# Kernel tuning notes

Measured on AMD Instinct MI355X. Metric: run time of the kernel, lower is better.

Reference implementation:

```python
import jax, jax.numpy as jnp
import numpy as np

F, P, H, HEADS, C, NCLS = 18, 128, 256, 8, 32, 625
SCALES = (2, 4, 6)
MAX_ITER = 2  # self.max_iterations in the source


def _mhsa(x, Wq, bq, Wk, bk, Wv, bv, Wo, bo):
    # x: [B, S, H]. Adjacency mask is all-ones in the source (adjacency()
    # returns torch.ones), so the mask is a mathematical no-op and is omitted.
    B, S, _ = x.shape
    hd = H // HEADS
    q = (x @ Wq + bq).reshape(B, S, HEADS, hd)
    k = (x @ Wk + bk).reshape(B, S, HEADS, hd)
    v = (x @ Wv + bv).reshape(B, S, HEADS, hd)
    scores = jnp.einsum('bqhd,bkhd->bhqk', q, k) / jnp.sqrt(jnp.float32(hd))
    attn = jax.nn.softmax(scores, axis=-1)
    out = jnp.einsum('bhqk,bkhd->bqhd', attn, v).reshape(B, S, H)
    return out @ Wo + bo


def _temporal_locality(scale, emb, Wq, bq, Wk, bk, Wv, bv, Wo, bo):
    # Vectorized overlap-add version of the python loop over windows.
    nw = F - scale + 1
    idx = jnp.arange(nw)[:, None] + jnp.arange(scale)[None, :]   # [nw, scale]
    windows = emb[idx].reshape(nw, scale * P, H)                 # [nw, s*P, H]
    out = _mhsa(windows, Wq, bq, Wk, bk, Wv, bv, Wo, bo)
    out = out.reshape(nw * scale, P, H)
    gval = jnp.zeros((F, P, H), emb.dtype).at[idx.reshape(-1)].add(out)
    # overlap counts == the hardcoded norm_scale vectors for F=18
    counts = jnp.zeros((F,), emb.dtype).at[idx.reshape(-1)].add(1.0)
    return gval / counts[:, None, None]


def _forward(multiscale_embed, unary_W, unary_b, halt_W, halt_b, compat,
             mp_W, mp_b, cls_W, cls_b,
             mhsa_Wq, mhsa_bq, mhsa_Wk, mhsa_bk,
             mhsa_Wv, mhsa_bv, mhsa_Wo, mhsa_bo):
    context = jnp.zeros_like(multiscale_embed)                 # [F, P, H]
    ptn = jnp.zeros((F,), multiscale_embed.dtype)
    Rt = jnp.zeros_like(ptn)
    Nt = jnp.zeros_like(ptn)
    # unary potentials: [F, P, C] -> permute -> [P, F, C]
    marginal = (multiscale_embed @ unary_W + unary_b).transpose(1, 0, 2)
    inputs = multiscale_embed                                   # [F, P, H]
    for _ in range(MAX_ITER):
        # --- halting probability (ACT-style) ---
        p = jnp.mean(jax.nn.sigmoid(inputs @ halt_W + halt_b), axis=1)[:, 0]  # [F]
        run = (ptn < 1.0).astype(ptn.dtype)
        new_halted = (ptn + p * run > 0.99).astype(ptn.dtype) * run
        run = (ptn + p * run <= 0.99).astype(ptn.dtype) * run
        ptn = ptn + p * run
        Rt = Rt + new_halted * (1.0 - ptn)
        ptn = ptn + new_halted * Rt
        Nt = Nt + run + new_halted
        # --- message passing: multi-scale windowed self-attention ---
        g = jnp.zeros_like(inputs)
        for i, s in enumerate(SCALES):
            g = g + _temporal_locality(s, inputs,
                                       mhsa_Wq[i], mhsa_bq[i], mhsa_Wk[i], mhsa_bk[i],
                                       mhsa_Wv[i], mhsa_bv[i], mhsa_Wo[i], mhsa_bo[i])
        temporal = 0.25 * g                                     # [F, P, H]
        inputs_p = temporal.transpose(1, 0, 2)                  # [P, F, H]
        pairwise = inputs_p @ mp_W + mp_b                       # [P, F, C]
        # compatibility transform: the chunk/cat reshuffle is an identity
        # permutation; the math is out_k = sum_c compat[k,c] * pairwise[...,c]
        pairwise = jnp.einsum('pfc,kc->pfk', pairwise, compat)
        marginal = marginal - pairwise
        # --- transition function ---
        w = (p * run + new_halted * Rt)[:, None, None]          # [F,1,1]
        inputs = inputs_p.transpose(1, 0, 2)                    # [F, P, H]
        context = inputs * w + context * (1.0 - w)
    # --- cluster features ---
    # chunk/cat flattening uses index order p*F + f on both tensors
    m = jax.nn.softmax(marginal, axis=2).reshape(P * F, C)
    ctx = context.transpose(1, 0, 2).reshape(P * F, H)
    cluster_features = m.T @ ctx                                # [C, H]
    classes = jnp.sum(cluster_features, axis=0, keepdims=True) @ cls_W + cls_b
    return classes                                              # [1, NCLS]


def setup_inputs() -> dict:
    key = jax.random.key(0)
    ks = jax.random.split(key, 16)
    init = lambda k, shape: jax.random.normal(k, shape, dtype=jnp.float32) * 0.02
    return {
        'multiscale_embed': jax.random.normal(ks[0], (F, P, H), dtype=jnp.float32),
        'unary_W': init(ks[1], (H, C)),
        'unary_b': jnp.zeros((C,), jnp.float32),
        'halt_W': init(ks[2], (H, 1)),
        'halt_b': jnp.ones((1,), jnp.float32),  # bias filled with 1.0 in source
        'compat': -jnp.eye(C, dtype=jnp.float32),
        'mp_W': init(ks[3], (H, C)),
        'mp_b': jnp.zeros((C,), jnp.float32),
        'cls_W': init(ks[4], (H, NCLS)),
        'cls_b': jnp.zeros((NCLS,), jnp.float32),
        'mhsa_Wq': init(ks[5], (3, H, H)),
        'mhsa_bq': jnp.zeros((3, H), jnp.float32),
        'mhsa_Wk': init(ks[6], (3, H, H)),
        'mhsa_bk': jnp.zeros((3, H), jnp.float32),
        'mhsa_Wv': init(ks[7], (3, H, H)),
        'mhsa_bv': jnp.zeros((3, H), jnp.float32),
        'mhsa_Wo': init(ks[8], (3, H, H)),
        'mhsa_bo': jnp.zeros((3, H), jnp.float32),
        'labels': jax.random.randint(ks[9], (1,), 0, NCLS),
    }


def reference(multiscale_embed, unary_W, unary_b, halt_W, halt_b, compat,
              mp_W, mp_b, cls_W, cls_b,
              mhsa_Wq, mhsa_bq, mhsa_Wk, mhsa_bk,
              mhsa_Wv, mhsa_bv, mhsa_Wo, mhsa_bo, labels):
    del labels  # labels are not used in the forward math shown in the source
    return _forward(multiscale_embed, unary_W, unary_b, halt_W, halt_b, compat,
                    mp_W, mp_b, cls_W, cls_b,
                    mhsa_Wq, mhsa_bq, mhsa_Wk, mhsa_bk,
                    mhsa_Wv, mhsa_bv, mhsa_Wo, mhsa_bo)
```

## Files before the change

kernel.cpp:

```cpp
#include <hip/hip_runtime.h>
#include <hip/hip_bf16.h>

typedef __hip_bfloat16 bf16;

#define F 18
#define P 128
#define H 256
#define HEADS 8
#define HD 32
#define NCLS 625
#define FPH (F*P*H)
#define RPS 589824
#define NT16 144

#define OF_PTN    16
#define OF_RT     48
#define OF_W      80
#define OF_OSUM   128
#define OF_CTX    512
#define OF_FW     (OF_CTX + FPH)
#define WO2_HALTW 0
#define WO2_HALTB 256
#define WO2_CLSB  272
#define WO2_CLSW  912
#define WO2_BQ    160912
#define WO2_BK    161680
#define WO2_BV    162448
#define WO2_BO    163216
#define FW_TOTAL  163984
#define NF_TOTAL  (OF_FW + FW_TOTAL)

#define BB_WQT 0
#define BB_WKT 196608
#define BB_WVT 393216
#define BB_WOT 589824
#define BB_INP 786432
#define BB_QB  1376256
#define BB_KB  (BB_QB + 3*RPS)
#define BB_VT  (BB_KB + 3*RPS)
#define BB_AO  (BB_VT + 3*RPS)
#define BB_OB  (BB_AO + 3*RPS)
#define OB_ROWS0 0
#define OB_ROWS1 4352
#define OB_ROWS2 12032

typedef __attribute__((ext_vector_type(8))) short s8v;
typedef __attribute__((ext_vector_type(4))) short s4v;
typedef __attribute__((ext_vector_type(4))) float f4v;

__device__ __forceinline__ float b2f(bf16 x){ return __bfloat162float(x); }
__device__ __forceinline__ unsigned short f2bu(float x){
    union { __hip_bfloat16 h; unsigned short u; } cv; cv.h = __float2bfloat16(x); return cv.u;
}
__device__ __forceinline__ float bu2f(unsigned short u){
    union { unsigned int x; float f; } cv; cv.x = ((unsigned int)u) << 16; return cv.f;
}
__device__ __forceinline__ void b2x2(unsigned int u, float& a, float& b){
    union { unsigned int x; float f; } c1, c2;
    c1.x = u << 16; c2.x = u & 0xffff0000u; a = c1.f; b = c2.f;
}

#if __has_builtin(__builtin_amdgcn_cvt_pk_bf16_f32)
typedef __attribute__((ext_vector_type(2))) __bf16 bf2_t;
__device__ __forceinline__ unsigned int pk2(float a, float b){
    union { bf2_t v; unsigned int u; } cv;
    cv.v = __builtin_amdgcn_cvt_pk_bf16_f32(a, b);
    return cv.u;
}
#else
__device__ __forceinline__ unsigned int pk2(float a, float b){
    return (unsigned int)f2bu(a) | ((unsigned int)f2bu(b) << 16);
}
#endif

#if __has_builtin(__builtin_amdgcn_exp2f)
__device__ __forceinline__ float fexp2(float x){ return __builtin_amdgcn_exp2f(x); }
#else
__device__ __forceinline__ float fexp2(float x){ return exp2f(x); }
#endif

__device__ __forceinline__ int imin(int a,int b){ return a<b?a:b; }
__device__ __forceinline__ int imax(int a,int b){ return a>b?a:b; }

__device__ __forceinline__ int detect_bf16_block(const unsigned int* __restrict__ embw,
                                                 int* scnt)
{
    if (threadIdx.x == 0) *scnt = 0;
    __syncthreads();
    int c = 0;
    {
        unsigned int e = (embw[2*threadIdx.x] >> 7) & 0xffu;
        if (e >= 120u && e <= 130u) c++;
        e = (embw[2*threadIdx.x + 1] >> 7) & 0xffu;
        if (e >= 120u && e <= 130u) c++;
    }
    atomicAdd(scnt, c);
    __syncthreads();
    return (*scnt > 256) ? 1 : 0;
}

struct ConvArgs {
    const void* src[13];
    int mode[13];
    int n[13];
    int off[13];
};
__global__ __launch_bounds__(256) void k_convert(ConvArgs a,
        const unsigned int* __restrict__ embw,
        float* __restrict__ ws, bf16* __restrict__ bb)
{
    __shared__ int scnt;
    const int isbf = detect_bf16_block(embw, &scnt);
    int gid = blockIdx.x*256 + threadIdx.x;
#pragma unroll
    for (int t = 0; t < 13; ++t){
        if (gid < a.n[t]){
            float v = isbf ? b2f(((const bf16*)a.src[t])[gid])
                           : ((const float*)a.src[t])[gid];
            if (a.mode[t] == 0){
                ws[a.off[t] + gid] = v;
            } else if (a.mode[t] == 1){
                const int i = gid >> 16, rem = gid & 65535;
                const int k = rem >> 8, nn = rem & 255;
                bb[a.off[t] + (i << 16) + (nn << 8) + k] = __float2bfloat16(v);
            } else {
                bb[BB_INP + gid] = __float2bfloat16(v);
            }
            return;
        }
        gid -= a.n[t];
    }
}

__global__ __launch_bounds__(256) void k_qkv_mfma(const bf16* __restrict__ X,
        const bf16* __restrict__ WQT, const bf16* __restrict__ WKT,
        const bf16* __restrict__ WVT, const float* __restrict__ fw,
        bf16* __restrict__ qball, bf16* __restrict__ kball, bf16* __restrict__ vball)
{
    const int tid = threadIdx.x;
    if (blockIdx.z == 3){
        if (blockIdx.x >= F || blockIdx.y != 0) return;
        __shared__ float hw[H];
        __shared__ float red[256];
        float* ws = (float*)fw - OF_FW;
        const float* hW = fw + WO2_HALTW;
        const int f = blockIdx.x;
        hw[tid] = hW[tid];
        __syncthreads();
        float sg = 0.f;
        if (tid < P){
            const uint4* row = (const uint4*)(X + (size_t)(f*P + tid)*H);
            float acc = fw[WO2_HALTB];
#pragma unroll
            for (int i = 0; i < 16; ++i){
                const uint4 u = row[i];
                float a0,a1,a2,a3,a4,a5,a6,a7;
                b2x2(u.x,a0,a1); b2x2(u.y,a2,a3); b2x2(u.z,a4,a5); b2x2(u.w,a6,a7);
                const int b = i*16;
                acc = fmaf(a0,hw[b+0],acc); acc = fmaf(a1,hw[b+1],acc);
                acc = fmaf(a2,hw[b+2],acc); acc = fmaf(a3,hw[b+3],acc);
                acc = fmaf(a4,hw[b+4],acc); acc = fmaf(a5,hw[b+5],acc);
                acc = fmaf(a6,hw[b+6],acc); acc = fmaf(a7,hw[b+7],acc);
            }
            sg = 1.f/(1.f + __expf(-acc));
        }
        red[tid] = sg;
        __syncthreads();
        for (int s = 128; s > 0; s >>= 1){ if (tid < s) red[tid] += red[tid+s]; __syncthreads(); }
        if (tid == 0){
            float pf = red[0] * (1.f/P);
            float pt = ws[OF_PTN + f], rt = ws[OF_RT + f];
            float run  = (pt < 1.f) ? 1.f : 0.f;
            float cond = (pt + pf*run > 0.99f) ? 1.f : 0.f;
            float nh   = cond*run;
            run = (1.f - cond)*run;
            pt += pf*run;
            rt += nh*(1.f - pt);
            pt += nh*rt;
            ws[OF_PTN + f] = pt; ws[OF_RT + f] = rt;
            ws[OF_W   + f] = pf*run + nh*rt;
        }
        return;
    }
    const int wave = tid >> 6, lane = tid & 63;
    const int lq = lane & 15, quad = lane >> 4;
    const int m0 = blockIdx.x * 64;
    const int n0 = blockIdx.y * 64 + wave * 16;
    const int i  = blockIdx.z;
    const int wo = i << 16;

    const bf16* arow[4];
#pragma unroll
    for (int mt = 0; mt < 4; ++mt)
        arow[mt] = X + (size_t)(m0 + mt*16 + lq)*H + quad*8;
    const bf16* bqp = WQT + wo + (size_t)(n0 + lq)*H + quad*8;
    const bf16* bkp = WKT + wo + (size_t)(n0 + lq)*H + quad*8;
    const bf16* bvp = WVT + wo + (size_t)(n0 + lq)*H + quad*8;

    f4v aq[4], ak[4], av[4];
#pragma unroll
    for (int mt = 0; mt < 4; ++mt){
        aq[mt] = (f4v){0.f,0.f,0.f,0.f};
        ak[mt] = (f4v){0.f,0.f,0.f,0.f};
        av[mt] = (f4v){0.f,0.f,0.f,0.f};
    }
#pragma unroll
    for (int k0 = 0; k0 < H; k0 += 32){
        const s8v bfq = *(const s8v*)(bqp + k0);
        const s8v bfk = *(const s8v*)(bkp + k0);
        const s8v bfv = *(const s8v*)(bvp + k0);
#pragma unroll
        for (int mt = 0; mt < 4; ++mt){
            const s8v af = *(const s8v*)(arow[mt] + k0);
            aq[mt] = __builtin_amdgcn_mfma_f32_16x16x32_bf16(bfq, af, aq[mt], 0, 0, 0);
            ak[mt] = __builtin_amdgcn_mfma_f32_16x16x32_bf16(bfk, af, ak[mt], 0, 0, 0);
            av[mt] = __builtin_amdgcn_mfma_f32_16x16x32_bf16(af, bfv, av[mt], 0, 0, 0);
        }
    }
    bf16* qo = qball + (size_t)i*RPS;
    bf16* ko = kball + (size_t)i*RPS;
    bf16* vo = vball + (size_t)i*RPS;

    const int cbase = n0 + 4*quad;
    const float4 bq4 = *(const float4*)(fw + WO2_BQ + i*256 + cbase);
    const float4 bk4 = *(const float4*)(fw + WO2_BK + i*256 + cbase);
    const int h2q  = cbase >> 5;
    const int dimq = (cbase >> 3) & 3;
    const int j2b  = cbase & 7;
    const int colv = n0 + lq;
    const float bvv = fw[WO2_BV + i*256 + colv];
    const int h2v = colv >> 5;
    const int half = (colv >> 4) & 1;
    const int lqv  = colv & 15;
#pragma unroll
    for (int mt = 0; mt < 4; ++mt){
        const int t16 = (m0 >> 4) + mt;
        const size_t qkidx = ((size_t)(h2q*NT16 + t16)*64 + lq + 16*dimq)*8 + j2b;
        uint2 qst, kst;
        qst.x = pk2(aq[mt][0] + bq4.x, aq[mt][1] + bq4.y);
        qst.y = pk2(aq[mt][2] + bq4.z, aq[mt][3] + bq4.w);
        kst.x = pk2(ak[mt][0] + bk4.x, ak[mt][1] + bk4.y);
        kst.y = pk2(ak[mt][2] + bk4.z, ak[mt][3] + bk4.w);
        *(uint2*)(qo + qkidx) = qst;
        *(uint2*)(ko + qkidx) = kst;
        const size_t vbase = ((size_t)(h2v*NT16 + t16)*64 + lqv + 16*quad)*8 + half*4;
        uint2 vst;
        vst.x = pk2(av[mt][0] + bvv, av[mt][1] + bvv);
        vst.y = pk2(av[mt][2] + bvv, av[mt][3] + bvv);
        *(uint2*)(vo + vbase) = vst;
    }
}

#if __has_builtin(__builtin_amdgcn_mfma_f32_16x16x16bf16_1k)
#define ATTN_HAVE_1K 1
#else
#define ATTN_HAVE_1K 0
#endif

__global__ __launch_bounds__(256) void k_attn_fused(const bf16* __restrict__ qball,
        const bf16* __restrict__ kball, const bf16* __restrict__ vball,
        bf16* __restrict__ obuf)
{
    const int bid = blockIdx.x;
    int i, rel, s, nw, nqt, obase;
    if (bid < 1248)      { i = 2; rel = bid;        s = 6; nw = 13; nqt = 12; obase = OB_ROWS2; }
    else if (bid < 2208) { i = 1; rel = bid - 1248; s = 4; nw = 15; nqt = 8;  obase = OB_ROWS1; }
    else                 { i = 0; rel = bid - 2208; s = 2; nw = 17; nqt = 4;  obase = OB_ROWS0; }
    const int S = nqt << 6;
    const int qt = rel % nqt;
    const int rest = rel / nqt;
    const int h = rest & 7;
    const int w = rest >> 3;

    const bf16* qs = qball + (size_t)i*RPS;
    const bf16* ks = kball + (size_t)i*RPS;
    const bf16* vs = vball + (size_t)i*RPS;

    const int tid = threadIdx.x;
    const int wave = tid >> 6, lane = tid & 63;
    const int lq = lane & 15, quad = lane >> 4;

    const int qt16 = w*8 + qt*4 + wave;
    s8v qf;
    {
        const float SCL2 = 0.17677669529663687f * 1.4426950408889634f;
        union { s8v v; unsigned int u[4]; } qin, qsc;
        qin.v = *(const s8v*)(qs + ((size_t)(h*NT16 + qt16)*64 + lane)*8);
#pragma unroll
        for (int j = 0; j < 4; ++j){
            float a, b;
            b2x2(qin.u[j], a, b);
            qsc.u[j] = pk2(a*SCL2, b*SCL2);
        }
        qf = qsc.v;
    }

    float m = -3e38f, l = 0.f;
    f4v o0 = {0.f,0.f,0.f,0.f}, o1 = {0.f,0.f,0.f,0.f};

    for (int ch = 0; ch < s; ++ch){
        const int kt0 = w*8 + ch*8;
        f4v st[8];
#pragma unroll
        for (int tt = 0; tt < 4; ++tt){
            const s8v kf0 = *(const s8v*)(ks + ((size_t)(h*NT16 + kt0 + tt*2    )*64 + lane)*8);
            const s8v kf1 = *(const s8v*)(ks + ((size_t)(h*NT16 + kt0 + tt*2 + 1)*64 + lane)*8);
            f4v z = {0.f,0.f,0.f,0.f};
            st[2*tt]   = __builtin_amdgcn_mfma_f32_16x16x32_bf16(kf0, qf, z, 0, 0, 0);
            st[2*tt+1] = __builtin_amdgcn_mfma_f32_16x16x32_bf16(kf1, qf, z, 0, 0, 0);
        }
        union { uint4 q; s4v h2v[2]; } vA[4], vB[4];
#pragma unroll
        for (int tt = 0; tt < 4; ++tt){
            vA[tt].q = *(const uint4*)(vs + ((size_t)(h*NT16 + kt0 + tt*2    )*64 + lane)*8);
            vB[tt].q = *(const uint4*)(vs + ((size_t)(h*NT16 + kt0 + tt*2 + 1)*64 + lane)*8);
        }
        float mc = -3e38f;
#pragma unroll
        for (int t8 = 0; t8 < 8; ++t8)
            mc = fmaxf(mc, fmaxf(fmaxf(st[t8][0], st[t8][1]), fmaxf(st[t8][2], st[t8][3])));
        mc = fmaxf(mc, __shfl_xor(mc, 16));
        mc = fmaxf(mc, __shfl_xor(mc, 32));
        const float mn = fmaxf(m, mc);
        const float alpha = fexp2(m - mn);
        float ls = 0.f;
#pragma unroll
        for (int t8 = 0; t8 < 8; ++t8){
#pragma unroll
            for (int r = 0; r < 4; ++r){
                const float e = fexp2(st[t8][r] - mn);
                st[t8][r] = e;
                ls += e;
            }
        }
        ls += __shfl_xor(ls, 16);
        ls += __shfl_xor(ls, 32);
        l = l*alpha + ls;
        m = mn;
        o0 = o0 * alpha;
        o1 = o1 * alpha;

#pragma unroll
        for (int tt = 0; tt < 4; ++tt){
#if ATTN_HAVE_1K
            union { unsigned int u[2]; s4v v; } pf0, pf1;
            pf0.u[0] = pk2(st[2*tt][0],   st[2*tt][1]);
            pf0.u[1] = pk2(st[2*tt][2],   st[2*tt][3]);
            pf1.u[0] = pk2(st[2*tt+1][0], st[2*tt+1][1]);
            pf1.u[1] = pk2(st[2*tt+1][2], st[2*tt+1][3]);
            o0 = __builtin_amdgcn_mfma_f32_16x16x16bf16_1k(vA[tt].h2v[0], pf0.v, o0, 0, 0, 0);
            o0 = __builtin_amdgcn_mfma_f32_16x16x16bf16_1k(vB[tt].h2v[0], pf1.v, o0, 0, 0, 0);
            o1 = __builtin_amdgcn_mfma_f32_16x16x16bf16_1k(vA[tt].h2v[1], pf0.v, o1, 0, 0, 0);
            o1 = __builtin_amdgcn_mfma_f32_16x16x16bf16_1k(vB[tt].h2v[1], pf1.v, o1, 0, 0, 0);
#else
            union { s4v h2v[2]; s8v v; } va0, va1;
            va0.h2v[0] = vA[tt].h2v[0]; va0.h2v[1] = vB[tt].h2v[0];
            va1.h2v[0] = vA[tt].h2v[1]; va1.h2v[1] = vB[tt].h2v[1];
            const unsigned int p0x = pk2(st[2*tt][0],   st[2*tt][1]);
            const unsigned int p0y = pk2(st[2*tt][2],   st[2*tt][3]);
            const unsigned int p1x = pk2(st[2*tt+1][0], st[2*tt+1][1]);
            const unsigned int p1y = pk2(st[2*tt+1][2], st[2*tt+1][3]);
            const int srcA = lq + ((( quad<<1)      & 3) << 4);
            const int srcB = lq + ((((quad<<1) | 1) & 3) << 4);
            const unsigned int a0 = (unsigned int)__shfl((int)p0x, srcA);
            const unsigned int a1 = (unsigned int)__shfl((int)p0y, srcA);
            const unsigned int a2 = (unsigned int)__shfl((int)p0x, srcB);
            const unsigned int a3 = (unsigned int)__shfl((int)p0y, srcB);
            const unsigned int b0 = (unsigned int)__shfl((int)p1x, srcA);
            const unsigned int b1 = (unsigned int)__shfl((int)p1y, srcA);
            const unsigned int b2 = (unsigned int)__shfl((int)p1x, srcB);
            const unsigned int b3 = (unsigned int)__shfl((int)p1y, srcB);
            const bool hi = (quad >= 2);
            union { unsigned int u[4]; s8v v; } bfr;
            bfr.u[0] = hi ? b0 : a0; bfr.u[1] = hi ? b1 : a1;
            bfr.u[2] = hi ? b2 : a2; bfr.u[3] = hi ? b3 : a3;
            o0 = __builtin_amdgcn_mfma_f32_16x16x32_bf16(va0.v, bfr.v, o0, 0, 0, 0);
            o1 = __builtin_amdgcn_mfma_f32_16x16x32_bf16(va1.v, bfr.v, o1, 0, 0, 0);
#endif
        }
    }
    const int pos = qt*64 + wave*16 + lq;
    const int qrow = w*P + pos;
    const int fframe = qrow >> 7;
    const int cnt = imin(nw-1, fframe) - imax(0, fframe - s + 1) + 1;
    const float scl = 1.f / (l * (float)cnt);
    bf16* op = obuf + (size_t)(obase + w*S + pos)*H + h*HD;
    *(unsigned int*)(op + quad*4)          = pk2(o0[0]*scl, o0[1]*scl);
    *(unsigned int*)(op + quad*4 + 2)      = pk2(o0[2]*scl, o0[3]*scl);
    *(unsigned int*)(op + 16 + quad*4)     = pk2(o1[0]*scl, o1[1]*scl);
    *(unsigned int*)(op + 16 + quad*4 + 2) = pk2(o1[2]*scl, o1[3]*scl);
}

__global__ __launch_bounds__(256) void k_oadd(const bf16* __restrict__ obuf,
                                              bf16* __restrict__ aoall)
{
    const int r = blockIdx.x, i = blockIdx.y, c = threadIdx.x;
    int s, nw, obase;
    if (i == 0)      { s = 2; nw = 17; obase = OB_ROWS0; }
    else if (i == 1) { s = 4; nw = 15; obase = OB_ROWS1; }
    else             { s = 6; nw = 13; obase = OB_ROWS2; }
    const int S = s << 7;
    const int f = r >> 7, p = r & 127;
    const int wlo = imax(0, f - s + 1), whi = imin(nw - 1, f);
    float sum = 0.f;
    for (int w = wlo; w <= whi; ++w)
        sum += b2f(obuf[(size_t)(obase + w*S + (f - w)*P + p)*H + c]);
    const size_t idx = ((size_t)((r >> 4)*8 + (c >> 5))*64
                        + (r & 15) + 16*((c >> 3) & 3))*8 + (c & 7);
    aoall[(size_t)i*RPS + idx] = __float2bfloat16(sum);
}

__global__ __launch_bounds__(256) void k_oproj_trans(const bf16* __restrict__ aoall,
        const bf16* __restrict__ WOT, const float* __restrict__ ws,
        bf16* __restrict__ inpb, float* __restrict__ context)
{
    const int tid = threadIdx.x;
    const int wave = tid >> 6, lane = tid & 63;
    const int lq = lane & 15, quad = lane >> 4;
    const int m0 = blockIdx.x * 64;
    const int n0 = blockIdx.y * 64 + wave * 16;

    f4v acc[4];
#pragma unroll
    for (int mt = 0; mt < 4; ++mt) acc[mt] = (f4v){0.f,0.f,0.f,0.f};

    for (int i = 0; i < 3; ++i){
        const bf16* A = aoall + (size_t)i*RPS;
        const bf16* bp = WOT + (i<<16) + (size_t)(n0 + lq)*H + quad*8;
#pragma unroll
        for (int k0 = 0; k0 < H; k0 += 32){
            const s8v bf_ = *(const s8v*)(bp + k0);
#pragma unroll
            for (int mt = 0; mt < 4; ++mt){
                const s8v af = *(const s8v*)(A +
                    ((size_t)(((m0 >> 4) + mt)*8 + (k0 >> 5))*64 + lane)*8);
                acc[mt] = __builtin_amdgcn_mfma_f32_16x16x32_bf16(af, bf_, acc[mt], 0, 0, 0);
            }
        }
    }
    const int col = n0 + lq;
    const float bosum = ws[OF_FW + WO2_BO + col] + ws[OF_FW + WO2_BO + 256 + col]
                      + ws[OF_FW + WO2_BO + 512 + col];
#pragma unroll
    for (int mt = 0; mt < 4; ++mt){
#pragma unroll
        for (int r = 0; r < 4; ++r){
            const int row = m0 + mt*16 + quad*4 + r;
            const float tval = 0.25f * (acc[mt][r] + bosum);
            const float wf = ws[OF_W + (row >> 7)];
            const size_t idx = (size_t)row*H + col;
            inpb[idx] = __float2bfloat16(tval);
            context[idx] = tval*wf + context[idx]*(1.f - wf);
        }
    }
}

__global__ __launch_bounds__(256) void k_reduce(const float* __restrict__ context,
        float* __restrict__ osum)
{
    const int hcol = threadIdx.x;
    const float* base = context + (size_t)blockIdx.x * 64 * H;
    float s = 0.f;
#pragma unroll 8
    for (int r = 0; r < 64; ++r) s += base[(size_t)r*H + hcol];
    atomicAdd(&osum[hcol], s);
}

__global__ __launch_bounds__(256) void k_classes(const float* __restrict__ ws,
        const unsigned int* __restrict__ embw, void* __restrict__ out)
{
    __shared__ int scnt;
    __shared__ float os[H];
    const int isbf = detect_bf16_block(embw, &scnt);
    const int tid = threadIdx.x;
    os[tid] = ws[OF_OSUM + tid];
    __syncthreads();
    const int n = blockIdx.x*256 + tid;
    if (n < NCLS){
        const float* clsW = ws + OF_FW + WO2_CLSW;
        float acc = ws[OF_FW + WO2_CLSB + n];
        for (int hh = 0; hh < H; ++hh) acc = fmaf(os[hh], clsW[(size_t)hh*NCLS + n], acc);
        if (isbf) ((bf16*)out)[n] = __float2bfloat16(acc);
        else      ((float*)out)[n] = acc;
    }
}

extern "C" void kernel_launch(void* const* d_in, const int* in_sizes, int n_in,
                              void* d_out, int out_size, void* d_ws, size_t ws_size,
                              hipStream_t stream)
{
    (void)in_sizes; (void)n_in; (void)out_size; (void)ws_size;
    float* WS = (float*)d_ws;
    float* context = WS + OF_CTX;
    float* fw      = WS + OF_FW;
    bf16*  bb      = (bf16*)(WS + NF_TOTAL);
    bf16*  inpb    = bb + BB_INP;
    bf16*  qb      = bb + BB_QB;
    bf16*  kb      = bb + BB_KB;
    bf16*  vT      = bb + BB_VT;
    bf16*  ao      = bb + BB_AO;
    bf16*  ob      = bb + BB_OB;

    (void)hipMemsetAsync(WS, 0, (size_t)OF_FW*4, stream);

    ConvArgs ca;
    const int srcs[13]  = {0, 3, 4, 8, 9, 11, 13, 15, 17, 10, 12, 14, 16};
    const int modes[13] = {2, 0, 0, 0, 0, 0, 0, 0, 0, 1, 1, 1, 1};
    const int ns[13]    = {FPH, 256, 1, H*NCLS, NCLS, 768, 768, 768, 768,
                           196608, 196608, 196608, 196608};
    const int offs[13]  = {0,
        OF_FW+WO2_HALTW, OF_FW+WO2_HALTB, OF_FW+WO2_CLSW, OF_FW+WO2_CLSB,
        OF_FW+WO2_BQ, OF_FW+WO2_BK, OF_FW+WO2_BV, OF_FW+WO2_BO,
        BB_WQT, BB_WKT, BB_WVT, BB_WOT};
    int total = 0;
    for (int t = 0; t < 13; ++t){
        ca.src[t] = d_in[srcs[t]]; ca.mode[t] = modes[t];
        ca.n[t] = ns[t]; ca.off[t] = offs[t]; total += ns[t];
    }
    k_convert<<<(total + 255)/256, 256, 0, stream>>>(ca,
        (const unsigned int*)d_in[0], WS, bb);

    for (int it = 0; it < 2; ++it){
        k_qkv_mfma<<<dim3(36, 4, 4), 256, 0, stream>>>(inpb,
            bb+BB_WQT, bb+BB_WKT, bb+BB_WVT, fw, qb, kb, vT);
        k_attn_fused<<<2752, 256, 0, stream>>>(qb, kb, vT, ob);
        k_oadd<<<dim3(2304, 3), 256, 0, stream>>>(ob, ao);
        k_oproj_trans<<<dim3(36, 4), 256, 0, stream>>>(ao, bb+BB_WOT, WS,
            inpb, context);
    }
    k_reduce<<<36, 256, 0, stream>>>(context, WS + OF_OSUM);
    k_classes<<<3, 256, 0, stream>>>(WS, (const unsigned int*)d_in[0], d_out);
}
```

Baseline: 268.2 us.

## Share key-chunk scores across overlapping windows and fuse overlap-add into attention

Attention is reorganised per query frame instead of per window. Each 128-key frame chunk's scores, exponentials and PV product are computed once and merged into per-window online-softmax states for every window that contains both the query frame and that key chunk. The windows are then normalised and averaged in registers and written directly in the layout the output projection expects. This removes the intermediate per-window output buffer and the separate overlap-add kernel, and it avoids recomputing QK and PV for frames that appear in several overlapping windows. In exchange each thread keeps up to SS sets of accumulators, which raises register pressure, and only 864 blocks are launched instead of 2752.

```diff
diff --git a/kernel.cpp b/kernel.cpp
--- a/kernel.cpp
+++ b/kernel.cpp
@@ -39,10 +39,6 @@
 #define BB_KB  (BB_QB + 3*RPS)
 #define BB_VT  (BB_KB + 3*RPS)
 #define BB_AO  (BB_VT + 3*RPS)
-#define BB_OB  (BB_AO + 3*RPS)
-#define OB_ROWS0 0
-#define OB_ROWS1 4352
-#define OB_ROWS2 12032
 
 typedef __attribute__((ext_vector_type(8))) short s8v;
 typedef __attribute__((ext_vector_type(4))) short s4v;
@@ -257,30 +253,15 @@
 #define ATTN_HAVE_1K 0
 #endif
 
-__global__ __launch_bounds__(256) void k_attn_fused(const bf16* __restrict__ qball,
-        const bf16* __restrict__ kball, const bf16* __restrict__ vball,
-        bf16* __restrict__ obuf)
-{
-    const int bid = blockIdx.x;
-    int i, rel, s, nw, nqt, obase;
-    if (bid < 1248)      { i = 2; rel = bid;        s = 6; nw = 13; nqt = 12; obase = OB_ROWS2; }
-    else if (bid < 2208) { i = 1; rel = bid - 1248; s = 4; nw = 15; nqt = 8;  obase = OB_ROWS1; }
-    else                 { i = 0; rel = bid - 2208; s = 2; nw = 17; nqt = 4;  obase = OB_ROWS0; }
-    const int S = nqt << 6;
-    const int qt = rel % nqt;
-    const int rest = rel / nqt;
-    const int h = rest & 7;
-    const int w = rest >> 3;
-
-    const bf16* qs = qball + (size_t)i*RPS;
-    const bf16* ks = kball + (size_t)i*RPS;
-    const bf16* vs = vball + (size_t)i*RPS;
-
-    const int tid = threadIdx.x;
-    const int wave = tid >> 6, lane = tid & 63;
+template<int SS>
+__device__ __forceinline__ void attn_body(const bf16* __restrict__ qs,
+        const bf16* __restrict__ ks, const bf16* __restrict__ vs,
+        bf16* __restrict__ aos, int f, int h, int t, int lane)
+{
+    const int NW = F - SS + 1;
     const int lq = lane & 15, quad = lane >> 4;
-
-    const int qt16 = w*8 + qt*4 + wave;
+    const int qt16 = f*8 + t;
+
     s8v qf;
     {
         const float SCL2 = 0.17677669529663687f * 1.4426950408889634f;
@@ -295,11 +276,22 @@
         qf = qsc.v;
     }
 
-    float m = -3e38f, l = 0.f;
-    f4v o0 = {0.f,0.f,0.f,0.f}, o1 = {0.f,0.f,0.f,0.f};
-
-    for (int ch = 0; ch < s; ++ch){
-        const int kt0 = w*8 + ch*8;
+    const int wLo = imax(0, f - SS + 1);
+    const int wHi = imin(NW - 1, f);
+    const int cnt = wHi - wLo + 1;
+    const int gHi = wHi + SS - 1;
+
+    float mw[SS], lw[SS];
+    f4v ow0[SS], ow1[SS];
+#pragma unroll
+    for (int ws = 0; ws < SS; ++ws){
+        mw[ws] = -3e38f; lw[ws] = 0.f;
+        ow0[ws] = (f4v){0.f,0.f,0.f,0.f};
+        ow1[ws] = (f4v){0.f,0.f,0.f,0.f};
+    }
+
+    for (int g = wLo; g <= gHi; ++g){
+        const int kt0 = g*8;
         f4v st[8];
 #pragma unroll
         for (int tt = 0; tt < 4; ++tt){
@@ -315,31 +307,25 @@
             vA[tt].q = *(const uint4*)(vs + ((size_t)(h*NT16 + kt0 + tt*2    )*64 + lane)*8);
             vB[tt].q = *(const uint4*)(vs + ((size_t)(h*NT16 + kt0 + tt*2 + 1)*64 + lane)*8);
         }
-        float mc = -3e38f;
+        float mu = -3e38f;
 #pragma unroll
         for (int t8 = 0; t8 < 8; ++t8)
-            mc = fmaxf(mc, fmaxf(fmaxf(st[t8][0], st[t8][1]), fmaxf(st[t8][2], st[t8][3])));
-        mc = fmaxf(mc, __shfl_xor(mc, 16));
-        mc = fmaxf(mc, __shfl_xor(mc, 32));
-        const float mn = fmaxf(m, mc);
-        const float alpha = fexp2(m - mn);
-        float ls = 0.f;
+            mu = fmaxf(mu, fmaxf(fmaxf(st[t8][0], st[t8][1]), fmaxf(st[t8][2], st[t8][3])));
+        mu = fmaxf(mu, __shfl_xor(mu, 16));
+        mu = fmaxf(mu, __shfl_xor(mu, 32));
+        float Lg = 0.f;
 #pragma unroll
         for (int t8 = 0; t8 < 8; ++t8){
 #pragma unroll
             for (int r = 0; r < 4; ++r){
-                const float e = fexp2(st[t8][r] - mn);
+                const float e = fexp2(st[t8][r] - mu);
                 st[t8][r] = e;
-                ls += e;
+                Lg += e;
             }
         }
-        ls += __shfl_xor(ls, 16);
-        ls += __shfl_xor(ls, 32);
-        l = l*alpha + ls;
-        m = mn;
-        o0 = o0 * alpha;
-        o1 = o1 * alpha;
-
+        Lg += __shfl_xor(Lg, 16);
+        Lg += __shfl_xor(Lg, 32);
+        f4v P0 = {0.f,0.f,0.f,0.f}, P1 = {0.f,0.f,0.f,0.f};
 #pragma unroll
         for (int tt = 0; tt < 4; ++tt){
 #if ATTN_HAVE_1K
@@ -348,10 +334,10 @@
             pf0.u[1] = pk2(st[2*tt][2],   st[2*tt][3]);
             pf1.u[0] = pk2(st[2*tt+1][0], st[2*tt+1][1]);
             pf1.u[1] = pk2(st[2*tt+1][2], st[2*tt+1][3]);
-            o0 = __builtin_amdgcn_mfma_f32_16x16x16bf16_1k(vA[tt].h2v[0], pf0.v, o0, 0, 0, 0);
-            o0 = __builtin_amdgcn_mfma_f32_16x16x16bf16_1k(vB[tt].h2v[0], pf1.v, o0, 0, 0, 0);
-            o1 = __builtin_amdgcn_mfma_f32_16x16x16bf16_1k(vA[tt].h2v[1], pf0.v, o1, 0, 0, 0);
-            o1 = __builtin_amdgcn_mfma_f32_16x16x16bf16_1k(vB[tt].h2v[1], pf1.v, o1, 0, 0, 0);
+            P0 = __builtin_amdgcn_mfma_f32_16x16x16bf16_1k(vA[tt].h2v[0], pf0.v, P0, 0, 0, 0);
+            P0 = __builtin_amdgcn_mfma_f32_16x16x16bf16_1k(vB[tt].h2v[0], pf1.v, P0, 0, 0, 0);
+            P1 = __builtin_amdgcn_mfma_f32_16x16x16bf16_1k(vA[tt].h2v[1], pf0.v, P1, 0, 0, 0);
+            P1 = __builtin_amdgcn_mfma_f32_16x16x16bf16_1k(vB[tt].h2v[1], pf1.v, P1, 0, 0, 0);
 #else
             union { s4v h2v[2]; s8v v; } va0, va1;
             va0.h2v[0] = vA[tt].h2v[0]; va0.h2v[1] = vB[tt].h2v[0];
@@ -374,40 +360,73 @@
             union { unsigned int u[4]; s8v v; } bfr;
             bfr.u[0] = hi ? b0 : a0; bfr.u[1] = hi ? b1 : a1;
             bfr.u[2] = hi ? b2 : a2; bfr.u[3] = hi ? b3 : a3;
-            o0 = __builtin_amdgcn_mfma_f32_16x16x32_bf16(va0.v, bfr.v, o0, 0, 0, 0);
-            o1 = __builtin_amdgcn_mfma_f32_16x16x32_bf16(va1.v, bfr.v, o1, 0, 0, 0);
+            P0 = __builtin_amdgcn_mfma_f32_16x16x32_bf16(va0.v, bfr.v, P0, 0, 0, 0);
+            P1 = __builtin_amdgcn_mfma_f32_16x16x32_bf16(va1.v, bfr.v, P1, 0, 0, 0);
 #endif
         }
-    }
-    const int pos = qt*64 + wave*16 + lq;
-    const int qrow = w*P + pos;
-    const int fframe = qrow >> 7;
-    const int cnt = imin(nw-1, fframe) - imax(0, fframe - s + 1) + 1;
-    const float scl = 1.f / (l * (float)cnt);
-    bf16* op = obuf + (size_t)(obase + w*S + pos)*H + h*HD;
-    *(unsigned int*)(op + quad*4)          = pk2(o0[0]*scl, o0[1]*scl);
-    *(unsigned int*)(op + quad*4 + 2)      = pk2(o0[2]*scl, o0[3]*scl);
-    *(unsigned int*)(op + 16 + quad*4)     = pk2(o1[0]*scl, o1[1]*scl);
-    *(unsigned int*)(op + 16 + quad*4 + 2) = pk2(o1[2]*scl, o1[3]*scl);
-}
-
-__global__ __launch_bounds__(256) void k_oadd(const bf16* __restrict__ obuf,
-                                              bf16* __restrict__ aoall)
-{
-    const int r = blockIdx.x, i = blockIdx.y, c = threadIdx.x;
-    int s, nw, obase;
-    if (i == 0)      { s = 2; nw = 17; obase = OB_ROWS0; }
-    else if (i == 1) { s = 4; nw = 15; obase = OB_ROWS1; }
-    else             { s = 6; nw = 13; obase = OB_ROWS2; }
-    const int S = s << 7;
-    const int f = r >> 7, p = r & 127;
-    const int wlo = imax(0, f - s + 1), whi = imin(nw - 1, f);
-    float sum = 0.f;
-    for (int w = wlo; w <= whi; ++w)
-        sum += b2f(obuf[(size_t)(obase + w*S + (f - w)*P + p)*H + c]);
-    const size_t idx = ((size_t)((r >> 4)*8 + (c >> 5))*64
-                        + (r & 15) + 16*((c >> 3) & 3))*8 + (c & 7);
-    aoall[(size_t)i*RPS + idx] = __float2bfloat16(sum);
+#pragma unroll
+        for (int ws = 0; ws < SS; ++ws){
+            const int w = wLo + ws;
+            if (w <= wHi && w <= g && w >= g - SS + 1){
+                const float mn = fmaxf(mw[ws], mu);
+                const float a = fexp2(mw[ws] - mn);
+                const float b = fexp2(mu - mn);
+                lw[ws] = lw[ws]*a + Lg*b;
+#pragma unroll
+                for (int r = 0; r < 4; ++r){
+                    ow0[ws][r] = ow0[ws][r]*a + P0[r]*b;
+                    ow1[ws][r] = ow1[ws][r]*a + P1[r]*b;
+                }
+                mw[ws] = mn;
+            }
+        }
+    }
+    f4v acc0 = {0.f,0.f,0.f,0.f}, acc1 = {0.f,0.f,0.f,0.f};
+#pragma unroll
+    for (int ws = 0; ws < SS; ++ws){
+        if (ws < cnt){
+            const float inv = 1.f / (lw[ws] * (float)cnt);
+#pragma unroll
+            for (int r = 0; r < 4; ++r){
+                acc0[r] += ow0[ws][r]*inv;
+                acc1[r] += ow1[ws][r]*inv;
+            }
+        }
+    }
+    const int grp0 = (4*h + (quad >> 1)) & 3;
+    const int grp1 = (4*h + 2 + (quad >> 1)) & 3;
+    const int off  = 4*(quad & 1);
+    const size_t base = (size_t)(qt16*8 + h)*64;
+    uint2 s0, s1;
+    s0.x = pk2(acc0[0], acc0[1]); s0.y = pk2(acc0[2], acc0[3]);
+    s1.x = pk2(acc1[0], acc1[1]); s1.y = pk2(acc1[2], acc1[3]);
+    *(uint2*)(aos + (base + lq + 16*grp0)*8 + off) = s0;
+    *(uint2*)(aos + (base + lq + 16*grp1)*8 + off) = s1;
+}
+
+__global__ __launch_bounds__(256) void k_attn_fused(const bf16* __restrict__ qball,
+        const bf16* __restrict__ kball, const bf16* __restrict__ vball,
+        bf16* __restrict__ aoall)
+{
+    const int bid = blockIdx.x;
+    int i, rel;
+    if (bid < 288)      { i = 2; rel = bid; }
+    else if (bid < 576) { i = 1; rel = bid - 288; }
+    else                { i = 0; rel = bid - 576; }
+    const int f = rel >> 4;
+    const int rest = rel & 15;
+    const int h = rest >> 1;
+    const int wave = threadIdx.x >> 6, lane = threadIdx.x & 63;
+    const int t = (rest & 1)*4 + wave;
+
+    const bf16* qs = qball + (size_t)i*RPS;
+    const bf16* ks = kball + (size_t)i*RPS;
+    const bf16* vs = vball + (size_t)i*RPS;
+    bf16* aos = aoall + (size_t)i*RPS;
+
+    if (i == 2)      attn_body<6>(qs, ks, vs, aos, f, h, t, lane);
+    else if (i == 1) attn_body<4>(qs, ks, vs, aos, f, h, t, lane);
+    else             attn_body<2>(qs, ks, vs, aos, f, h, t, lane);
 }
 
 __global__ __launch_bounds__(256) void k_oproj_trans(const bf16* __restrict__ aoall,
@@ -499,7 +518,6 @@
     bf16*  kb      = bb + BB_KB;
     bf16*  vT      = bb + BB_VT;
     bf16*  ao      = bb + BB_AO;
-    bf16*  ob      = bb + BB_OB;
 
     (void)hipMemsetAsync(WS, 0, (size_t)OF_FW*4, stream);
 
@@ -523,8 +541,7 @@
     for (int it = 0; it < 2; ++it){
         k_qkv_mfma<<<dim3(36, 4, 4), 256, 0, stream>>>(inpb,
             bb+BB_WQT, bb+BB_WKT, bb+BB_WVT, fw, qb, kb, vT);
-        k_attn_fused<<<2752, 256, 0, stream>>>(qb, kb, vT, ob);
-        k_oadd<<<dim3(2304, 3), 256, 0, stream>>>(ob, ao);
+        k_attn_fused<<<864, 256, 0, stream>>>(qb, kb, vT, ao);
         k_oproj_trans<<<dim3(36, 4), 256, 0, stream>>>(ao, bb+BB_WOT, WS,
             inpb, context);
     }
```

Result: faster. 227.1 us (-15.3%).
